# Performance work log

Measured on AMD Instinct MI355X. Metric: run time of the kernel, lower is better.

## Reference

```python
import jax, jax.numpy as jnp
import numpy as np
from jax import lax

B, K = 16, 10
C_IN, C_OUT = 32, 64
H_IN, W_IN = 32, 32
KS, STRIDE, PAD = 3, 1, 1
H_OUT = (H_IN + 2 * PAD - KS) // STRIDE + 1
W_OUT = (W_IN + 2 * PAD - KS) // STRIDE + 1


def setup_inputs() -> dict:
    key = jax.random.key(0)
    k1, k2, k3 = jax.random.split(key, 3)
    x = jax.random.normal(k1, (B, K, C_IN, H_IN, W_IN), dtype=jnp.float32)
    # init_local (non-mono, non-first): std = 1/sqrt(0.5 * in_ch * k^2)
    std = 1.0 / np.sqrt(0.5 * C_IN * KS ** 2)
    weight = jax.random.normal(k2, (H_OUT, W_OUT, C_OUT, C_IN, KS, KS), dtype=jnp.float32) * std
    bias = jax.random.normal(k3, (K, C_OUT, H_OUT, W_OUT), dtype=jnp.float32) * 0.01
    return {"x": x, "weight": weight, "bias": bias}


def reference(x, weight, bias):
    # x: [B, K, C_in, H, W] -> merge batch and category dims
    b, k = x.shape[:2]
    xr = x.reshape((b * k,) + x.shape[2:])  # [BK, C_in, H, W]
    # Extract all kxk patches in one fused op: [BK, C_in*KS*KS, h_out, w_out]
    # feature dim ordered (c, kh, kw) -- matches weight layout [o, i, kh, kw].
    patches = lax.conv_general_dilated_patches(
        xr, filter_shape=(KS, KS), window_strides=(STRIDE, STRIDE),
        padding=[(PAD, PAD), (PAD, PAD)])
    w2 = weight.reshape(H_OUT, W_OUT, C_OUT, C_IN * KS * KS)  # [i, j, o, f]
    # Per-pixel unshared contraction (block-diagonal batched GEMM)
    out = jnp.einsum('bfij,ijof->boij', patches, w2)  # [BK, C_out, h_out, w_out]
    out = out.reshape(b, k, C_OUT, H_OUT, W_OUT)
    return out + bias[None]
```

## Files before the change

### kernel.cpp

```cpp
#include <hip/hip_runtime.h>


#define HW    32
#define CIN   32
#define COUT  64
#define FDIM  288
#define FPAD  296
#define NBK   160
#define HP    34
#define PLANE (NBK * CIN)
#define SLOT_SH (3 * PLANE)
#define WOFF  (4 * SLOT_SH)

using f32x4  = __attribute__((ext_vector_type(4))) float;
using bf16x8 = __attribute__((ext_vector_type(8))) short;
using s16x4  = __attribute__((ext_vector_type(4))) short;

static __device__ inline unsigned short f2bf(float f) {
    unsigned u = __float_as_uint(f);
    u += 0x7FFFu + ((u >> 16) & 1u);
    return (unsigned short)(u >> 16);
}
static __device__ inline void gl_lds16(const short* src, short* dst) {
    __builtin_amdgcn_global_load_lds(
        (const __attribute__((address_space(1))) unsigned int*)src,
        (__attribute__((address_space(3))) unsigned int*)dst, 16, 0, 0);
}
static constexpr size_t XC_BYTES = (size_t)HP * HP * PLANE * 2;
static constexpr size_t CO_BYTES = (size_t)1024 * COUT * NBK * 2;

__global__ __launch_bounds__(256) void hz_kernel(short* __restrict__ xc)
{
    const int id = blockIdx.x;
    int h, w;
    if (id < 34)      { h = 0;  w = id; }
    else if (id < 68) { h = 33; w = id - 34; }
    else { const int e = id - 68; h = 1 + (e >> 1); w = (e & 1) * 33; }
    uint2* p = reinterpret_cast<uint2*>(xc + (size_t)(h * HP + w) * PLANE);
    const uint2 z = {0u, 0u};
#pragma unroll
    for (int r = 0; r < 5; ++r)
        p[threadIdx.x + r * 256] = z;
}

__global__ __launch_bounds__(256) void t1_kernel(
    const float* __restrict__ x, short* __restrict__ xc)
{
    __shared__ short tile[HW][36];
    const int bid = blockIdx.x;
    const int bk  = bid >> 5;
    const int h   = bid & 31;
    const int tid = threadIdx.x;
    {
        const int c  = tid >> 3;
        const int w4 = (tid & 7) * 4;
        const float4 v = *reinterpret_cast<const float4*>(
            x + (size_t)(bk * 32 + c) * 1024 + h * 32 + w4);
        tile[w4 + 0][c] = (short)f2bf(v.x);
        tile[w4 + 1][c] = (short)f2bf(v.y);
        tile[w4 + 2][c] = (short)f2bf(v.z);
        tile[w4 + 3][c] = (short)f2bf(v.w);
    }
    __syncthreads();
    {
        const int w  = tid >> 3;
        const int cq = tid & 7;
        const uint2 pk = *reinterpret_cast<const uint2*>(&tile[w][cq * 4]);
        const int sidx = bk * 32 + ((cq * 4) ^ (((bk >> 1) & 3) << 3));
        *reinterpret_cast<uint2*>(
            xc + (size_t)((h + 1) * HP + (w + 1)) * PLANE + sidx) = pk;
    }
}

__global__ __launch_bounds__(512) void local2d_main_kernel(
    const short* __restrict__ xc,
    const float* __restrict__ w,
    short* __restrict__ co)
{
    __shared__ __align__(1024) short Sl[WOFF + COUT * FPAD];

    const int hb = blockIdx.x;
    const int lb = (hb & 7) * 32 + (hb >> 3);
    const int i  = lb >> 3;
    const int jt = lb & 7;
    const int j0 = jt * 4;
    const int tid = threadIdx.x;

    const int wave = tid >> 6;
    const int lane = tid & 63;
    const int nt   = wave & 3;
    const int mh   = wave >> 2;
    const int l15  = lane & 15;
    const int lg   = lane >> 4;
    const int lg8  = lg * 8;

    short* WL = Sl + WOFF;

    int rowbyte[5];
#pragma unroll
    for (int mt = 0; mt < 5; ++mt) {
        const int bk = mh * 80 + mt * 16 + l15;
        rowbyte[mt] = (bk * 64 + lg * 16) ^ (((bk >> 1) & 3) << 4);
    }

    float4 wv[9];
#define WLOAD(pp) {                                                        \
        const float* wp = w + (size_t)((i * 32) + j0 + (pp)) * (COUT * FDIM); \
        _Pragma("unroll")                                                  \
        for (int q = 0; q < 9; ++q) {                                      \
            const int g  = tid + q * 512;                                  \
            const int o2 = g / 72;                                         \
            const int f4 = (g - o2 * 72) * 4;                              \
            wv[q] = *reinterpret_cast<const float4*>(wp + o2 * FDIM + f4); \
        } }

    WLOAD(0)
    {
#pragma unroll
        for (int r = 0; r < 15; ++r) {
            const int u   = tid + r * 512;
            const int s   = u / 1920;
            const int rem = u - s * 1920;
            const int pl  = rem / 640;
            const int cu  = rem - pl * 640;
            const short* src = xc + (size_t)((i + pl) * HP + (j0 + s)) * PLANE + cu * 8;
            gl_lds16(src, Sl + (size_t)u * 8);
        }
    }

    const f32x4 z4 = {0.f, 0.f, 0.f, 0.f};

#pragma unroll
    for (int p = 0; p < 4; ++p) {
#pragma unroll
        for (int q = 0; q < 9; ++q) {
            const int g  = tid + q * 512;
            const int o2 = g / 72;
            const int f4 = (g - o2 * 72) * 4;
            const float vv[4] = {wv[q].x, wv[q].y, wv[q].z, wv[q].w};
            short* wrow = WL + o2 * FPAD;
#pragma unroll
            for (int e = 0; e < 4; ++e) {
                const int f = f4 + e; const int c = f / 9;
                const int cell = f - c * 9;
                wrow[cell * 32 + c] = (short)f2bf(vv[e]);
            }
        }
        __syncthreads();

        if (p < 3) WLOAD(p + 1)
        if (p == 1 || p == 2) {
            const int s  = p - 1;
            const int jw = j0 + 4 + s;
#pragma unroll
            for (int r = 0; r < 4; ++r) {
                const int u = tid + r * 512;
                if (u < 1920) {
                    const int pl = u / 640;
                    const int cu = u - pl * 640;
                    const short* src = xc + (size_t)((i + pl) * HP + jw) * PLANE + cu * 8;
                    gl_lds16(src, Sl + (size_t)(s * SLOT_SH) + (size_t)u * 8);
                }
            }
        }

        f32x4 acc0 = z4, acc1 = z4, acc2 = z4, acc3 = z4, acc4 = z4;
        const short* bp = WL + (nt * 16 + l15) * FPAD + lg8;
#pragma unroll
        for (int kc = 0; kc < 9; ++kc) {
            const int kh   = kc / 3;
            const int kw   = kc - kh * 3;
            const int slot = (p + kw) & 3;
            const char* ab = (const char*)Sl + slot * (SLOT_SH * 2) + kh * (PLANE * 2);
            const bf16x8 b = *reinterpret_cast<const bf16x8*>(bp + kc * 32);
            const bf16x8 a0 = *reinterpret_cast<const bf16x8*>(ab + rowbyte[0]);
            const bf16x8 a1 = *reinterpret_cast<const bf16x8*>(ab + rowbyte[1]);
            const bf16x8 a2 = *reinterpret_cast<const bf16x8*>(ab + rowbyte[2]);
            const bf16x8 a3 = *reinterpret_cast<const bf16x8*>(ab + rowbyte[3]);
            const bf16x8 a4 = *reinterpret_cast<const bf16x8*>(ab + rowbyte[4]);
            acc0 = __builtin_amdgcn_mfma_f32_16x16x32_bf16(a0, b, acc0, 0, 0, 0);
            acc1 = __builtin_amdgcn_mfma_f32_16x16x32_bf16(a1, b, acc1, 0, 0, 0);
            acc2 = __builtin_amdgcn_mfma_f32_16x16x32_bf16(a2, b, acc2, 0, 0, 0);
            acc3 = __builtin_amdgcn_mfma_f32_16x16x32_bf16(a3, b, acc3, 0, 0, 0);
            acc4 = __builtin_amdgcn_mfma_f32_16x16x32_bf16(a4, b, acc4, 0, 0, 0);
        }

        {
            const int pix = i * 32 + j0 + p;
            const int o3  = nt * 16 + l15;
            const size_t cb = ((size_t)pix * COUT + o3) * NBK + mh * 80 + lg * 4;
#define STORE1(a, mt) { s16x4 s_;                                          \
            s_.x = (short)f2bf(a[0]); s_.y = (short)f2bf(a[1]);            \
            s_.z = (short)f2bf(a[2]); s_.w = (short)f2bf(a[3]);            \
            *reinterpret_cast<s16x4*>(co + cb + (mt) * 16) = s_; }
            STORE1(acc0, 0) STORE1(acc1, 1) STORE1(acc2, 2)
            STORE1(acc3, 3) STORE1(acc4, 4)
#undef STORE1
        }
        __syncthreads();
    }
#undef WLOAD
}

__global__ __launch_bounds__(256) void t2_kernel(
    const short* __restrict__ co,
    const float* __restrict__ bias,
    float* __restrict__ out)
{
    __shared__ short tl[32][36];
    const int b    = blockIdx.x;
    const int o    = b & 63;
    const int rest = b >> 6;
    const int bkT  = rest % 5;
    const int pixT = rest / 5;
    const int tid  = threadIdx.x;
    {
        const int p  = tid >> 3;
        const int bq = tid & 7;
        const int pix = pixT * 32 + p;
        const s16x4 v = *reinterpret_cast<const s16x4*>(
            co + ((size_t)pix * COUT + o) * NBK + bkT * 32 + bq * 4);
        *reinterpret_cast<s16x4*>(&tl[p][bq * 4]) = v;
    }
    __syncthreads();
    {
        const int bb = tid >> 3;
        const int pq = tid & 7;
        const int bk = bkT * 32 + bb;
        const int k  = bk % 10;
        const size_t pbase = (size_t)pixT * 32 + pq * 4;
        const float4 bv = *reinterpret_cast<const float4*>(
            bias + ((size_t)(k * COUT + o) << 10) + pbase);
        float4 r;
        r.x = __uint_as_float(((unsigned)(unsigned short)tl[pq * 4 + 0][bb]) << 16) + bv.x;
        r.y = __uint_as_float(((unsigned)(unsigned short)tl[pq * 4 + 1][bb]) << 16) + bv.y;
        r.z = __uint_as_float(((unsigned)(unsigned short)tl[pq * 4 + 2][bb]) << 16) + bv.z;
        r.w = __uint_as_float(((unsigned)(unsigned short)tl[pq * 4 + 3][bb]) << 16) + bv.w;
        *reinterpret_cast<float4*>(out + ((size_t)(bk * COUT + o) << 10) + pbase) = r;
    }
}

__global__ __launch_bounds__(256) void xpose_kernel(
    const float* __restrict__ x, short* __restrict__ xc)
{
    __shared__ short tile[HW][36];
    const int bid = blockIdx.x;
    const int bk  = bid >> 5;
    const int h   = bid & 31;
    const int tid = threadIdx.x;
    {
        const int c  = tid >> 3;
        const int w4 = (tid & 7) * 4;
        const float4 v = *reinterpret_cast<const float4*>(
            x + (size_t)(bk * 32 + c) * 1024 + h * 32 + w4);
        tile[w4 + 0][c] = (short)f2bf(v.x);
        tile[w4 + 1][c] = (short)f2bf(v.y);
        tile[w4 + 2][c] = (short)f2bf(v.z);
        tile[w4 + 3][c] = (short)f2bf(v.w);
    }
    __syncthreads();
    {
        const int w  = tid >> 3;
        const int cq = tid & 7;
        const uint2 pk = *reinterpret_cast<const uint2*>(&tile[w][cq * 4]);
        *reinterpret_cast<uint2*>(
            xc + ((size_t)(bk * 1024 + h * 32 + w) * 32 + cq * 4)) = pk;
    }
}

__global__ __launch_bounds__(512, 4) void local2d_mfma2_kernel(
    const short* __restrict__ xc,
    const float* __restrict__ w,
    const float* __restrict__ bias,
    float* __restrict__ out)
{
    __shared__ short Wl[COUT * FPAD];
    const int hb  = blockIdx.x;
    const int lb  = (hb & 7) * 128 + (hb >> 3);
    const int i   = lb >> 5;
    const int j   = lb & 31;
    const int pix = i * HW + j;
    const int tid = threadIdx.x;
    {
        const float* wp = w + (size_t)pix * (COUT * FDIM);
#pragma unroll
        for (int p = 0; p < 9; ++p) {
            const int g  = tid + p * 512;
            const int o  = g / 72;
            const int f4 = (g - o * 72) * 4;
            const float4 v = *reinterpret_cast<const float4*>(wp + o * FDIM + f4);
            const float vv[4] = {v.x, v.y, v.z, v.w};
            short* wrow = &Wl[o * FPAD];
#pragma unroll
            for (int e = 0; e < 4; ++e) {
                const int f    = f4 + e;
                const int c    = f / 9;
                const int cell = f - c * 9;
                wrow[cell * 32 + c] = (short)f2bf(vv[e]);
            }
        }
    }
    __syncthreads();
    const int wave = tid >> 6;
    const int lane = tid & 63;
    const int nt   = wave & 3;
    const int mh   = wave >> 2;
    const int l15  = lane & 15;
    const int lg8  = (lane >> 4) * 8;
    f32x4 acc[5];
#pragma unroll
    for (int mt = 0; mt < 5; ++mt)
#pragma unroll
        for (int r = 0; r < 4; ++r) acc[mt][r] = 0.f;
    const short* xb[5];
#pragma unroll
    for (int mt = 0; mt < 5; ++mt) {
        const int bk = mh * 80 + mt * 16 + l15;
        xb[mt] = xc + (size_t)bk * (HW * HW * CIN) + lg8;
    }
    const short* bp = &Wl[(nt * 16 + l15) * FPAD + lg8];
#pragma unroll
    for (int kc = 0; kc < 9; ++kc) {
        const int kh = kc / 3;
        const int kw = kc - kh * 3;
        const int ih = i - 1 + kh;
        const int jw = j - 1 + kw;
        if ((unsigned)ih >= (unsigned)HW || (unsigned)jw >= (unsigned)HW)
            continue;
        const bf16x8 b = *reinterpret_cast<const bf16x8*>(bp + kc * 32);
        const int xoff = (ih * HW + jw) * CIN;
#pragma unroll
        for (int mt = 0; mt < 5; ++mt) {
            const bf16x8 a = *reinterpret_cast<const bf16x8*>(xb[mt] + xoff);
            acc[mt] = __builtin_amdgcn_mfma_f32_16x16x32_bf16(a, b, acc[mt], 0, 0, 0);
        }
    }
    const int o  = nt * 16 + l15;
    const int r0 = (lane >> 4) * 4;
#pragma unroll
    for (int mt = 0; mt < 5; ++mt) {
        const int bk0 = mh * 80 + mt * 16 + r0;
#pragma unroll
        for (int r = 0; r < 4; ++r) {
            const int bk = bk0 + r;
            const int k  = bk % 10;
            out[((size_t)(bk * COUT + o) << 10) + pix] =
                acc[mt][r] + bias[((size_t)(k * COUT + o) << 10) + pix];
        }
    }
}

extern "C" void kernel_launch(void* const* d_in, const int* in_sizes, int n_in,
                              void* d_out, int out_size, void* d_ws, size_t ws_size,
                              hipStream_t stream) {
    const float* x    = (const float*)d_in[0];
    const float* w    = (const float*)d_in[1];
    const float* bias = (const float*)d_in[2];
    float* out        = (float*)d_out;

    if (ws_size >= XC_BYTES + CO_BYTES) {
        short* xc = (short*)d_ws;
        short* co = (short*)((char*)d_ws + XC_BYTES);
        hipLaunchKernelGGL(hz_kernel, dim3(132), dim3(256), 0, stream, xc);
        hipLaunchKernelGGL(t1_kernel, dim3(5120), dim3(256), 0, stream, x, xc);
        hipLaunchKernelGGL(local2d_main_kernel, dim3(256), dim3(512), 0, stream,
                           xc, w, co);
        hipLaunchKernelGGL(t2_kernel, dim3(10240), dim3(256), 0, stream,
                           co, bias, out);
    } else {
        short* xc = (short*)d_ws;
        hipLaunchKernelGGL(xpose_kernel, dim3(5120), dim3(256), 0, stream, x, xc);
        hipLaunchKernelGGL(local2d_mfma2_kernel, dim3(1024), dim3(512), 0, stream,
                           xc, w, bias, out);
    }
}
```

Measured before the change: 52.44 us.

## Double-buffer weight registers and hand-schedule waits in main local conv kernel

Unrolls the four-pixel loop of the main MFMA kernel by hand. Weight prefetch now uses two register buffers so the next pixel's weights are issued while the current ones are scattered to LDS. Explicit vmcnt/lgkmcnt waits, raw s_barrier and sched_barriers replace __syncthreads, so each wait covers only the loads actually needed. Input-slot prefetch is spread over 480 threads. This targets exposed global-load latency and barrier overhead, at the cost of more registers and fragile manual waitcnt accounting.

```diff
diff --git a/kernel.cpp b/kernel.cpp
--- a/kernel.cpp
+++ b/kernel.cpp
@@ -72,7 +72,14 @@
     }
 }
 
-__global__ __launch_bounds__(512) void local2d_main_kernel(
+#define SB()  __builtin_amdgcn_sched_barrier(0)
+#define VM(n) { asm volatile("s_waitcnt vmcnt(" #n ")" ::: "memory"); SB(); }
+#define LG0BAR() { asm volatile("s_waitcnt lgkmcnt(0)" ::: "memory"); SB(); \
+                   __builtin_amdgcn_s_barrier(); SB(); }
+#define BARA() { asm volatile("s_waitcnt lgkmcnt(0)" ::: "memory"); SB(); \
+                 __builtin_amdgcn_s_barrier(); SB(); }
+
+__global__ __launch_bounds__(512) void local2d_p_kernel(
     const short* __restrict__ xc,
     const float* __restrict__ w,
     short* __restrict__ co)
@@ -103,18 +110,88 @@
         rowbyte[mt] = (bk * 64 + lg * 16) ^ (((bk >> 1) & 3) << 4);
     }
 
-    float4 wv[9];
-#define WLOAD(pp) {                                                        \
+    float4 wv0[9], wv1[9];
+    const f32x4 z4 = {0.f, 0.f, 0.f, 0.f};
+    f32x4 acc0, acc1, acc2, acc3, acc4;
+
+#define WISSUE(dst, pp) {                                                  \
         const float* wp = w + (size_t)((i * 32) + j0 + (pp)) * (COUT * FDIM); \
         _Pragma("unroll")                                                  \
         for (int q = 0; q < 9; ++q) {                                      \
             const int g  = tid + q * 512;                                  \
             const int o2 = g / 72;                                         \
             const int f4 = (g - o2 * 72) * 4;                              \
-            wv[q] = *reinterpret_cast<const float4*>(wp + o2 * FDIM + f4); \
+            dst[q] = *reinterpret_cast<const float4*>(wp + o2 * FDIM + f4);\
+        } SB(); }
+
+#define SCATTER(src) {                                                     \
+        _Pragma("unroll")                                                  \
+        for (int q = 0; q < 9; ++q) {                                      \
+            const int g  = tid + q * 512;                                  \
+            const int o2 = g / 72;                                         \
+            const int f4 = (g - o2 * 72) * 4;                              \
+            const float vv[4] = {src[q].x, src[q].y, src[q].z, src[q].w};  \
+            short* wrow = WL + o2 * FPAD;                                  \
+            _Pragma("unroll")                                              \
+            for (int e = 0; e < 4; ++e) {                                  \
+                const int f = f4 + e; const int c = f / 9;                 \
+                const int cell = f - c * 9;                                \
+                wrow[cell * 32 + c] = (short)f2bf(vv[e]); } } SB(); }
+
+#define RISSUE(s) {                                                        \
+        if (tid < 480) {                                                   \
+            _Pragma("unroll")                                              \
+            for (int r = 0; r < 4; ++r) {                                  \
+                const int u  = tid + r * 480;                              \
+                const int pl = u / 640;                                    \
+                const int cu = u - pl * 640;                               \
+                const short* src = xc + (size_t)((i + pl) * HP + (j0 + 4 + (s))) * PLANE + cu * 8; \
+                gl_lds16(src, Sl + (size_t)((s) * SLOT_SH) + (size_t)u * 8); \
+            } } SB(); }
+
+#define COMPUTE(p) {                                                       \
+        acc0 = z4; acc1 = z4; acc2 = z4; acc3 = z4; acc4 = z4;             \
+        const short* bp = WL + (nt * 16 + l15) * FPAD + lg8;               \
+        _Pragma("unroll")                                                  \
+        for (int kc = 0; kc < 9; ++kc) {                                   \
+            const int kh   = kc / 3;                                       \
+            const int kw   = kc - kh * 3;                                  \
+            const int slot = ((p) + kw) & 3;                               \
+            const char* ab = (const char*)Sl + slot * (SLOT_SH * 2) + kh * (PLANE * 2); \
+            const bf16x8 b  = *reinterpret_cast<const bf16x8*>(bp + kc * 32); \
+            const bf16x8 a0 = *reinterpret_cast<const bf16x8*>(ab + rowbyte[0]); \
+            const bf16x8 a1 = *reinterpret_cast<const bf16x8*>(ab + rowbyte[1]); \
+            const bf16x8 a2 = *reinterpret_cast<const bf16x8*>(ab + rowbyte[2]); \
+            const bf16x8 a3 = *reinterpret_cast<const bf16x8*>(ab + rowbyte[3]); \
+            const bf16x8 a4 = *reinterpret_cast<const bf16x8*>(ab + rowbyte[4]); \
+            acc0 = __builtin_amdgcn_mfma_f32_16x16x32_bf16(a0, b, acc0, 0, 0, 0); \
+            acc1 = __builtin_amdgcn_mfma_f32_16x16x32_bf16(a1, b, acc1, 0, 0, 0); \
+            acc2 = __builtin_amdgcn_mfma_f32_16x16x32_bf16(a2, b, acc2, 0, 0, 0); \
+            acc3 = __builtin_amdgcn_mfma_f32_16x16x32_bf16(a3, b, acc3, 0, 0, 0); \
+            acc4 = __builtin_amdgcn_mfma_f32_16x16x32_bf16(a4, b, acc4, 0, 0, 0); \
         } }
 
-    WLOAD(0)
+#define STORE(p) {                                                         \
+        const int pix = i * 32 + j0 + (p);                                 \
+        const int o3  = nt * 16 + l15;                                     \
+        const size_t cb = ((size_t)pix * COUT + o3) * NBK + mh * 80 + lg * 4; \
+        { s16x4 s_; s_.x = (short)f2bf(acc0[0]); s_.y = (short)f2bf(acc0[1]); \
+          s_.z = (short)f2bf(acc0[2]); s_.w = (short)f2bf(acc0[3]);        \
+          *reinterpret_cast<s16x4*>(co + cb + 0) = s_; }                   \
+        { s16x4 s_; s_.x = (short)f2bf(acc1[0]); s_.y = (short)f2bf(acc1[1]); \
+          s_.z = (short)f2bf(acc1[2]); s_.w = (short)f2bf(acc1[3]);        \
+          *reinterpret_cast<s16x4*>(co + cb + 16) = s_; }                  \
+        { s16x4 s_; s_.x = (short)f2bf(acc2[0]); s_.y = (short)f2bf(acc2[1]); \
+          s_.z = (short)f2bf(acc2[2]); s_.w = (short)f2bf(acc2[3]);        \
+          *reinterpret_cast<s16x4*>(co + cb + 32) = s_; }                  \
+        { s16x4 s_; s_.x = (short)f2bf(acc3[0]); s_.y = (short)f2bf(acc3[1]); \
+          s_.z = (short)f2bf(acc3[2]); s_.w = (short)f2bf(acc3[3]);        \
+          *reinterpret_cast<s16x4*>(co + cb + 48) = s_; }                  \
+        { s16x4 s_; s_.x = (short)f2bf(acc4[0]); s_.y = (short)f2bf(acc4[1]); \
+          s_.z = (short)f2bf(acc4[2]); s_.w = (short)f2bf(acc4[3]);        \
+          *reinterpret_cast<s16x4*>(co + cb + 64) = s_; } }
+
+    WISSUE(wv0, 0)
     {
 #pragma unroll
         for (int r = 0; r < 15; ++r) {
@@ -126,80 +203,45 @@
             const short* src = xc + (size_t)((i + pl) * HP + (j0 + s)) * PLANE + cu * 8;
             gl_lds16(src, Sl + (size_t)u * 8);
         }
-    }
-
-    const f32x4 z4 = {0.f, 0.f, 0.f, 0.f};
-
-#pragma unroll
-    for (int p = 0; p < 4; ++p) {
-#pragma unroll
-        for (int q = 0; q < 9; ++q) {
-            const int g  = tid + q * 512;
-            const int o2 = g / 72;
-            const int f4 = (g - o2 * 72) * 4;
-            const float vv[4] = {wv[q].x, wv[q].y, wv[q].z, wv[q].w};
-            short* wrow = WL + o2 * FPAD;
-#pragma unroll
-            for (int e = 0; e < 4; ++e) {
-                const int f = f4 + e; const int c = f / 9;
-                const int cell = f - c * 9;
-                wrow[cell * 32 + c] = (short)f2bf(vv[e]);
-            }
-        }
-        __syncthreads();
-
-        if (p < 3) WLOAD(p + 1)
-        if (p == 1 || p == 2) {
-            const int s  = p - 1;
-            const int jw = j0 + 4 + s;
-#pragma unroll
-            for (int r = 0; r < 4; ++r) {
-                const int u = tid + r * 512;
-                if (u < 1920) {
-                    const int pl = u / 640;
-                    const int cu = u - pl * 640;
-                    const short* src = xc + (size_t)((i + pl) * HP + jw) * PLANE + cu * 8;
-                    gl_lds16(src, Sl + (size_t)(s * SLOT_SH) + (size_t)u * 8);
-                }
-            }
-        }
-
-        f32x4 acc0 = z4, acc1 = z4, acc2 = z4, acc3 = z4, acc4 = z4;
-        const short* bp = WL + (nt * 16 + l15) * FPAD + lg8;
-#pragma unroll
-        for (int kc = 0; kc < 9; ++kc) {
-            const int kh   = kc / 3;
-            const int kw   = kc - kh * 3;
-            const int slot = (p + kw) & 3;
-            const char* ab = (const char*)Sl + slot * (SLOT_SH * 2) + kh * (PLANE * 2);
-            const bf16x8 b = *reinterpret_cast<const bf16x8*>(bp + kc * 32);
-            const bf16x8 a0 = *reinterpret_cast<const bf16x8*>(ab + rowbyte[0]);
-            const bf16x8 a1 = *reinterpret_cast<const bf16x8*>(ab + rowbyte[1]);
-            const bf16x8 a2 = *reinterpret_cast<const bf16x8*>(ab + rowbyte[2]);
-            const bf16x8 a3 = *reinterpret_cast<const bf16x8*>(ab + rowbyte[3]);
-            const bf16x8 a4 = *reinterpret_cast<const bf16x8*>(ab + rowbyte[4]);
-            acc0 = __builtin_amdgcn_mfma_f32_16x16x32_bf16(a0, b, acc0, 0, 0, 0);
-            acc1 = __builtin_amdgcn_mfma_f32_16x16x32_bf16(a1, b, acc1, 0, 0, 0);
-            acc2 = __builtin_amdgcn_mfma_f32_16x16x32_bf16(a2, b, acc2, 0, 0, 0);
-            acc3 = __builtin_amdgcn_mfma_f32_16x16x32_bf16(a3, b, acc3, 0, 0, 0);
-            acc4 = __builtin_amdgcn_mfma_f32_16x16x32_bf16(a4, b, acc4, 0, 0, 0);
-        }
-
-        {
-            const int pix = i * 32 + j0 + p;
-            const int o3  = nt * 16 + l15;
-            const size_t cb = ((size_t)pix * COUT + o3) * NBK + mh * 80 + lg * 4;
-#define STORE1(a, mt) { s16x4 s_;                                          \
-            s_.x = (short)f2bf(a[0]); s_.y = (short)f2bf(a[1]);            \
-            s_.z = (short)f2bf(a[2]); s_.w = (short)f2bf(a[3]);            \
-            *reinterpret_cast<s16x4*>(co + cb + (mt) * 16) = s_; }
-            STORE1(acc0, 0) STORE1(acc1, 1) STORE1(acc2, 2)
-            STORE1(acc3, 3) STORE1(acc4, 4)
-#undef STORE1
-        }
-        __syncthreads();
-    }
-#undef WLOAD
+        SB();
+    }
+    VM(15)
+    SCATTER(wv0)
+    WISSUE(wv1, 1)
+    VM(9)
+    LG0BAR()
+
+    COMPUTE(0) STORE(0)
+    BARA()
+    VM(0)
+    SCATTER(wv1)
+    WISSUE(wv0, 2)
+    LG0BAR()
+
+    RISSUE(0)
+    COMPUTE(1) STORE(1)
+    BARA()
+    VM(4)
+    SCATTER(wv0)
+    WISSUE(wv1, 3)
+    VM(9)
+    LG0BAR()
+
+    RISSUE(1)
+    COMPUTE(2) STORE(2)
+    BARA()
+    VM(4)
+    SCATTER(wv1)
+    VM(0)
+    LG0BAR()
+
+    COMPUTE(3) STORE(3)
+
+#undef WISSUE
+#undef SCATTER
+#undef RISSUE
+#undef COMPUTE
+#undef STORE
 }
 
 __global__ __launch_bounds__(256) void t2_kernel(
@@ -363,7 +405,7 @@
         short* co = (short*)((char*)d_ws + XC_BYTES);
         hipLaunchKernelGGL(hz_kernel, dim3(132), dim3(256), 0, stream, xc);
         hipLaunchKernelGGL(t1_kernel, dim3(5120), dim3(256), 0, stream, x, xc);
-        hipLaunchKernelGGL(local2d_main_kernel, dim3(256), dim3(512), 0, stream,
+        hipLaunchKernelGGL(local2d_p_kernel, dim3(256), dim3(512), 0, stream,
                            xc, w, co);
         hipLaunchKernelGGL(t2_kernel, dim3(10240), dim3(256), 0, stream,
                            co, bias, out);
```

New measurement: 51.09 us. 2.6% less time.

## Prepack weights into MFMA layout and fuse bias epilogue into main GEMM kernel

Applied to the files above, without the earlier changes.

Adds a t3 kernel that converts the per-pixel weights to bf16 and stores them pre-permuted in the MFMA B-fragment order. The new main kernel reads A and B fragments straight from global memory into registers, with no LDS staging of the activation planes. Each wave accumulates a 5x4 tile of MFMA outputs for one pixel. The bias add and final transpose are fused in through an LDS column buffer, which removes the intermediate bf16 output buffer and the separate t2 pass. The cost is an extra weight-packing pass and heavy register use for the accumulators, and the path needs enough workspace to hold the packed weights.

```diff
diff --git a/kernel.cpp b/kernel.cpp
--- a/kernel.cpp
+++ b/kernel.cpp
@@ -11,6 +11,8 @@
 #define PLANE (NBK * CIN)
 #define SLOT_SH (3 * PLANE)
 #define WOFF  (4 * SLOT_SH)
+#define WPK   18432
+#define BKP   162
 
 using f32x4  = __attribute__((ext_vector_type(4))) float;
 using bf16x8 = __attribute__((ext_vector_type(8))) short;
@@ -21,12 +23,16 @@
     u += 0x7FFFu + ((u >> 16) & 1u);
     return (unsigned short)(u >> 16);
 }
+static __device__ inline float bf2f(short h) {
+    return __uint_as_float(((unsigned)(unsigned short)h) << 16);
+}
 static __device__ inline void gl_lds16(const short* src, short* dst) {
     __builtin_amdgcn_global_load_lds(
         (const __attribute__((address_space(1))) unsigned int*)src,
         (__attribute__((address_space(3))) unsigned int*)dst, 16, 0, 0);
 }
 static constexpr size_t XC_BYTES = (size_t)HP * HP * PLANE * 2;
+static constexpr size_t WP_BYTES = (size_t)1024 * WPK * 2;
 static constexpr size_t CO_BYTES = (size_t)1024 * COUT * NBK * 2;
 
 __global__ __launch_bounds__(256) void hz_kernel(short* __restrict__ xc)
@@ -43,7 +49,7 @@
         p[threadIdx.x + r * 256] = z;
 }
 
-__global__ __launch_bounds__(256) void t1_kernel(
+__global__ __launch_bounds__(256) void t1l_kernel(
     const float* __restrict__ x, short* __restrict__ xc)
 {
     __shared__ short tile[HW][36];
@@ -66,26 +72,188 @@
         const int w  = tid >> 3;
         const int cq = tid & 7;
         const uint2 pk = *reinterpret_cast<const uint2*>(&tile[w][cq * 4]);
+        *reinterpret_cast<uint2*>(
+            xc + (size_t)((h + 1) * HP + (w + 1)) * PLANE + bk * CIN + cq * 4) = pk;
+    }
+}
+
+__global__ __launch_bounds__(256) void t3_kernel(
+    const float* __restrict__ w, short* __restrict__ wpack)
+{
+    __shared__ short Wl[COUT * FPAD];
+    const int pix = blockIdx.x;
+    const int tid = threadIdx.x;
+
+    {
+        const float* wp = w + (size_t)pix * (COUT * FDIM);
+#pragma unroll
+        for (int q = 0; q < 18; ++q) {
+            const int g  = tid + q * 256;
+            const int o  = g / 72;
+            const int f4 = (g - o * 72) * 4;
+            const float4 v = *reinterpret_cast<const float4*>(wp + o * FDIM + f4);
+            const float vv[4] = {v.x, v.y, v.z, v.w};
+            short* wrow = &Wl[o * FPAD];
+#pragma unroll
+            for (int e = 0; e < 4; ++e) {
+                const int f = f4 + e;
+                const int c = f / 9;
+                const int cell = f - c * 9;
+                wrow[cell * 32 + c] = (short)f2bf(vv[e]);
+            }
+        }
+    }
+    __syncthreads();
+    {
+        short* dst = wpack + (size_t)pix * WPK;
+#pragma unroll
+        for (int q = 0; q < 9; ++q) {
+            const int u    = tid + q * 256;
+            const int kc   = u >> 8;
+            const int rem  = u & 255;
+            const int nt   = rem >> 6;
+            const int lane = rem & 63;
+            const int l15  = lane & 15;
+            const int lg   = lane >> 4;
+            const s16x4* src = reinterpret_cast<const s16x4*>(
+                &Wl[(nt * 16 + l15) * FPAD + kc * 32 + lg * 8]);
+            *reinterpret_cast<s16x4*>(dst + (size_t)u * 8 + 0) = src[0];
+            *reinterpret_cast<s16x4*>(dst + (size_t)u * 8 + 4) = src[1];
+        }
+    }
+}
+
+__global__ __launch_bounds__(512) void local2d_f_kernel(
+    const short* __restrict__ xc,
+    const short* __restrict__ wpack,
+    const float* __restrict__ bias,
+    float* __restrict__ out)
+{
+    __shared__ short col[4 * COUT * BKP];
+
+    const int hb = blockIdx.x;
+    const int i  = (hb & 7) * 4 + (hb >> 6);
+    const int jt = (hb >> 3) & 7;
+    const int j0 = jt * 4;
+    const int tid = threadIdx.x;
+
+    const int wave = tid >> 6;
+    const int lane = tid & 63;
+    const int p    = wave >> 1;
+    const int mh   = wave & 1;
+    const int l15  = lane & 15;
+    const int lg   = lane >> 4;
+    const int lg8  = lg * 8;
+    const int j    = j0 + p;
+    const int pix  = i * 32 + j;
+
+    const short* xbase = xc + ((size_t)i * HP + j) * PLANE
+                            + (mh * 80 + l15) * CIN + lg8;
+    const short* wpb = wpack + (size_t)pix * WPK + lane * 8;
+
+    f32x4 acc[5][4];
+#pragma unroll
+    for (int mt = 0; mt < 5; ++mt)
+#pragma unroll
+        for (int nt = 0; nt < 4; ++nt)
+#pragma unroll
+            for (int r = 0; r < 4; ++r) acc[mt][nt][r] = 0.f;
+
+#pragma unroll
+    for (int kc = 0; kc < 9; ++kc) {
+        const int kh = kc / 3;
+        const int kw = kc - kh * 3;
+        const short* ap = xbase + (kh * HP + kw) * PLANE;
+        bf16x8 a[5];
+#pragma unroll
+        for (int mt = 0; mt < 5; ++mt)
+            a[mt] = *reinterpret_cast<const bf16x8*>(ap + mt * 512);
+        bf16x8 b[4];
+#pragma unroll
+        for (int nt = 0; nt < 4; ++nt)
+            b[nt] = *reinterpret_cast<const bf16x8*>(wpb + (kc * 4 + nt) * 512);
+#pragma unroll
+        for (int nt = 0; nt < 4; ++nt)
+#pragma unroll
+            for (int mt = 0; mt < 5; ++mt)
+                acc[mt][nt] = __builtin_amdgcn_mfma_f32_16x16x32_bf16(
+                    a[mt], b[nt], acc[mt][nt], 0, 0, 0);
+    }
+
+#pragma unroll
+    for (int nt = 0; nt < 4; ++nt) {
+        const int o = nt * 16 + l15;
+#pragma unroll
+        for (int mt = 0; mt < 5; ++mt) {
+            s16x4 s;
+            s.x = (short)f2bf(acc[mt][nt][0]); s.y = (short)f2bf(acc[mt][nt][1]);
+            s.z = (short)f2bf(acc[mt][nt][2]); s.w = (short)f2bf(acc[mt][nt][3]);
+            *reinterpret_cast<s16x4*>(
+                &col[(p * COUT + o) * BKP + mh * 80 + mt * 16 + lg * 4]) = s;
+        }
+    }
+    __syncthreads();
+
+    const int pix0 = i * 32 + j0;
+#pragma unroll
+    for (int s = 0; s < 20; ++s) {
+        const int id = tid + s * 512;
+        const int o  = id & 63;
+        const int bk = id >> 6;
+        const int k  = bk % 10;
+        const float4 bv = *reinterpret_cast<const float4*>(
+            bias + (((size_t)(k * COUT + o)) << 10) + pix0);
+        float4 r;
+        r.x = bf2f(col[(0 * COUT + o) * BKP + bk]) + bv.x;
+        r.y = bf2f(col[(1 * COUT + o) * BKP + bk]) + bv.y;
+        r.z = bf2f(col[(2 * COUT + o) * BKP + bk]) + bv.z;
+        r.w = bf2f(col[(3 * COUT + o) * BKP + bk]) + bv.w;
+        *reinterpret_cast<float4*>(
+            out + (((size_t)(bk * COUT + o)) << 10) + pix0) = r;
+    }
+}
+
+__global__ __launch_bounds__(256) void t1s_kernel(
+    const float* __restrict__ x, short* __restrict__ xc)
+{
+    __shared__ short tile[HW][36];
+    const int bid = blockIdx.x;
+    const int bk  = bid >> 5;
+    const int h   = bid & 31;
+    const int tid = threadIdx.x;
+    {
+        const int c  = tid >> 3;
+        const int w4 = (tid & 7) * 4;
+        const float4 v = *reinterpret_cast<const float4*>(
+            x + (size_t)(bk * 32 + c) * 1024 + h * 32 + w4);
+        tile[w4 + 0][c] = (short)f2bf(v.x);
+        tile[w4 + 1][c] = (short)f2bf(v.y);
+        tile[w4 + 2][c] = (short)f2bf(v.z);
+        tile[w4 + 3][c] = (short)f2bf(v.w);
+    }
+    __syncthreads();
+    {
+        const int w  = tid >> 3;
+        const int cq = tid & 7;
+        const uint2 pk = *reinterpret_cast<const uint2*>(&tile[w][cq * 4]);
         const int sidx = bk * 32 + ((cq * 4) ^ (((bk >> 1) & 3) << 3));
         *reinterpret_cast<uint2*>(
             xc + (size_t)((h + 1) * HP + (w + 1)) * PLANE + sidx) = pk;
     }
 }
 
-__global__ __launch_bounds__(512) void local2d_main_kernel(
+__global__ __launch_bounds__(512) void local2d_m_kernel(
     const short* __restrict__ xc,
     const float* __restrict__ w,
     short* __restrict__ co)
 {
     __shared__ __align__(1024) short Sl[WOFF + COUT * FPAD];
-
     const int hb = blockIdx.x;
     const int lb = (hb & 7) * 32 + (hb >> 3);
     const int i  = lb >> 3;
     const int jt = lb & 7;
     const int j0 = jt * 4;
     const int tid = threadIdx.x;
-
     const int wave = tid >> 6;
     const int lane = tid & 63;
     const int nt   = wave & 3;
@@ -93,18 +261,15 @@
     const int l15  = lane & 15;
     const int lg   = lane >> 4;
     const int lg8  = lg * 8;
-
     short* WL = Sl + WOFF;
-
     int rowbyte[5];
 #pragma unroll
     for (int mt = 0; mt < 5; ++mt) {
         const int bk = mh * 80 + mt * 16 + l15;
         rowbyte[mt] = (bk * 64 + lg * 16) ^ (((bk >> 1) & 3) << 4);
     }
-
     float4 wv[9];
-#define WLOAD(pp) {                                                        \
+#define WLOADM(pp) {                                                       \
         const float* wp = w + (size_t)((i * 32) + j0 + (pp)) * (COUT * FDIM); \
         _Pragma("unroll")                                                  \
         for (int q = 0; q < 9; ++q) {                                      \
@@ -113,8 +278,7 @@
             const int f4 = (g - o2 * 72) * 4;                              \
             wv[q] = *reinterpret_cast<const float4*>(wp + o2 * FDIM + f4); \
         } }
-
-    WLOAD(0)
+    WLOADM(0)
     {
 #pragma unroll
         for (int r = 0; r < 15; ++r) {
@@ -127,9 +291,7 @@
             gl_lds16(src, Sl + (size_t)u * 8);
         }
     }
-
     const f32x4 z4 = {0.f, 0.f, 0.f, 0.f};
-
 #pragma unroll
     for (int p = 0; p < 4; ++p) {
 #pragma unroll
@@ -147,8 +309,7 @@
             }
         }
         __syncthreads();
-
-        if (p < 3) WLOAD(p + 1)
+        if (p < 3) WLOADM(p + 1)
         if (p == 1 || p == 2) {
             const int s  = p - 1;
             const int jw = j0 + 4 + s;
@@ -163,7 +324,6 @@
                 }
             }
         }
-
         f32x4 acc0 = z4, acc1 = z4, acc2 = z4, acc3 = z4, acc4 = z4;
         const short* bp = WL + (nt * 16 + l15) * FPAD + lg8;
 #pragma unroll
@@ -172,7 +332,7 @@
             const int kw   = kc - kh * 3;
             const int slot = (p + kw) & 3;
             const char* ab = (const char*)Sl + slot * (SLOT_SH * 2) + kh * (PLANE * 2);
-            const bf16x8 b = *reinterpret_cast<const bf16x8*>(bp + kc * 32);
+            const bf16x8 b  = *reinterpret_cast<const bf16x8*>(bp + kc * 32);
             const bf16x8 a0 = *reinterpret_cast<const bf16x8*>(ab + rowbyte[0]);
             const bf16x8 a1 = *reinterpret_cast<const bf16x8*>(ab + rowbyte[1]);
             const bf16x8 a2 = *reinterpret_cast<const bf16x8*>(ab + rowbyte[2]);
@@ -184,22 +344,20 @@
             acc3 = __builtin_amdgcn_mfma_f32_16x16x32_bf16(a3, b, acc3, 0, 0, 0);
             acc4 = __builtin_amdgcn_mfma_f32_16x16x32_bf16(a4, b, acc4, 0, 0, 0);
         }
-
         {
             const int pix = i * 32 + j0 + p;
             const int o3  = nt * 16 + l15;
             const size_t cb = ((size_t)pix * COUT + o3) * NBK + mh * 80 + lg * 4;
-#define STORE1(a, mt) { s16x4 s_;                                          \
+#define ST1(a, mt) { s16x4 s_;                                             \
             s_.x = (short)f2bf(a[0]); s_.y = (short)f2bf(a[1]);            \
             s_.z = (short)f2bf(a[2]); s_.w = (short)f2bf(a[3]);            \
             *reinterpret_cast<s16x4*>(co + cb + (mt) * 16) = s_; }
-            STORE1(acc0, 0) STORE1(acc1, 1) STORE1(acc2, 2)
-            STORE1(acc3, 3) STORE1(acc4, 4)
-#undef STORE1
+            ST1(acc0, 0) ST1(acc1, 1) ST1(acc2, 2) ST1(acc3, 3) ST1(acc4, 4)
+#undef ST1
         }
         __syncthreads();
     }
-#undef WLOAD
+#undef WLOADM
 }
 
 __global__ __launch_bounds__(256) void t2_kernel(
@@ -232,10 +390,10 @@
         const float4 bv = *reinterpret_cast<const float4*>(
             bias + ((size_t)(k * COUT + o) << 10) + pbase);
         float4 r;
-        r.x = __uint_as_float(((unsigned)(unsigned short)tl[pq * 4 + 0][bb]) << 16) + bv.x;
-        r.y = __uint_as_float(((unsigned)(unsigned short)tl[pq * 4 + 1][bb]) << 16) + bv.y;
-        r.z = __uint_as_float(((unsigned)(unsigned short)tl[pq * 4 + 2][bb]) << 16) + bv.z;
-        r.w = __uint_as_float(((unsigned)(unsigned short)tl[pq * 4 + 3][bb]) << 16) + bv.w;
+        r.x = bf2f(tl[pq * 4 + 0][bb]) + bv.x;
+        r.y = bf2f(tl[pq * 4 + 1][bb]) + bv.y;
+        r.z = bf2f(tl[pq * 4 + 2][bb]) + bv.z;
+        r.w = bf2f(tl[pq * 4 + 3][bb]) + bv.w;
         *reinterpret_cast<float4*>(out + ((size_t)(bk * COUT + o) << 10) + pbase) = r;
     }
 }
@@ -358,12 +516,20 @@
     const float* bias = (const float*)d_in[2];
     float* out        = (float*)d_out;
 
-    if (ws_size >= XC_BYTES + CO_BYTES) {
+    if (ws_size >= XC_BYTES + WP_BYTES) {
+        short* xc    = (short*)d_ws;
+        short* wpack = (short*)((char*)d_ws + XC_BYTES);
+        hipLaunchKernelGGL(hz_kernel, dim3(132), dim3(256), 0, stream, xc);
+        hipLaunchKernelGGL(t1l_kernel, dim3(5120), dim3(256), 0, stream, x, xc);
+        hipLaunchKernelGGL(t3_kernel, dim3(1024), dim3(256), 0, stream, w, wpack);
+        hipLaunchKernelGGL(local2d_f_kernel, dim3(256), dim3(512), 0, stream,
+                           xc, wpack, bias, out);
+    } else if (ws_size >= XC_BYTES + CO_BYTES) {
         short* xc = (short*)d_ws;
         short* co = (short*)((char*)d_ws + XC_BYTES);
         hipLaunchKernelGGL(hz_kernel, dim3(132), dim3(256), 0, stream, xc);
-        hipLaunchKernelGGL(t1_kernel, dim3(5120), dim3(256), 0, stream, x, xc);
-        hipLaunchKernelGGL(local2d_main_kernel, dim3(256), dim3(512), 0, stream,
+        hipLaunchKernelGGL(t1s_kernel, dim3(5120), dim3(256), 0, stream, x, xc);
+        hipLaunchKernelGGL(local2d_m_kernel, dim3(256), dim3(512), 0, stream,
                            xc, w, co);
         hipLaunchKernelGGL(t2_kernel, dim3(10240), dim3(256), 0, stream,
                            co, bias, out);
```

Measured after the change: 67.91 us. 1.3x slower.
